# Optimization experiments

Measured on AMD Instinct MI355X. Metric: run time of the kernel, lower is better.

## Reference

```python
import jax, jax.numpy as jnp
import numpy as np

NUM_TASKS = 8
NUM_EXPERTS = 8
TOPK = 2
WEX = 0.01
N_TOKENS = 4194304


def setup_inputs() -> dict:
    key = jax.random.key(0)
    k1, k2 = jax.random.split(key)
    router_logits = jax.random.normal(k1, (N_TOKENS, NUM_EXPERTS), dtype=jnp.float32)
    router_labels = jax.random.randint(k2, (N_TOKENS,), 0, NUM_TASKS, dtype=jnp.int64)
    return {"router_logits": router_logits, "router_labels": router_labels}


def reference(router_logits, router_labels):
    # call_update: detached softmax over experts
    probs = jax.lax.stop_gradient(
        jax.nn.softmax(router_logits.astype(jnp.float32), axis=-1)
    )  # [N, E]
    labels = router_labels.astype(jnp.int32)
    # Torch loop `for task in router_labels` adds segment_sum[task] once per
    # occurrence of task -> EX_task_gate[t] = count[t] * segment_sum[t]
    seg_sum = jax.ops.segment_sum(probs, labels, num_segments=NUM_TASKS)  # [T, E]
    counts = jax.ops.segment_sum(
        jnp.ones((probs.shape[0],), dtype=jnp.float32), labels, num_segments=NUM_TASKS
    )  # [T]
    EX_gate = seg_sum * counts[:, None]  # [T, E]
    # calculate_mutual_information_loss
    tot = EX_gate.sum() / TOPK
    EX_gate = EX_gate / (tot + 0.0001)
    P_TI = EX_gate.sum(axis=1, keepdims=True) + 0.0001  # [T, 1]
    P_EI = EX_gate.sum(axis=0, keepdims=True) + 0.0001  # [1, E]
    expert_loss = -(EX_gate * jnp.log(EX_gate / P_TI / P_EI + 0.0001)).sum()
    return jnp.float32(WEX) * expert_loss
```

## Files before the change

kernel.cpp:

```cpp
#include <hip/hip_runtime.h>
#include <hip/hip_bf16.h>

#define N_TOKENS    4194304
#define NUM_EXPERTS 8
#define NUM_TASKS   8
#define GRID        2048
#define BLOCK       256
#define NTH         (GRID * BLOCK)
#define HSLOTS      (N_TOKENS * 2 / NTH)
#define PF          4

__global__ __launch_bounds__(BLOCK) void mi_reduce_kernel(
    const float* __restrict__ logits,
    const int*   __restrict__ labels,
    float*       __restrict__ partials) {

  float acc[NUM_TASKS][4];
#pragma unroll
  for (int t = 0; t < NUM_TASKS; ++t)
#pragma unroll
    for (int e = 0; e < 4; ++e) acc[t][e] = 0.0f;

  const int u    = blockIdx.x * BLOCK + threadIdx.x;
  const int tok0 = u >> 1;
  const float4* __restrict__ lp = reinterpret_cast<const float4*>(logits);

  float4 va[PF]; int la[PF];
  float4 vb[PF]; int lb[PF];

#define LOADB(ARR, LARR, B)                                                  \
  _Pragma("unroll")                                                          \
  for (int j = 0; j < PF; ++j) {                                             \
    const int k = (B) * PF + j;                                              \
    (ARR)[j]  = lp[(size_t)k * NTH + u];            \
    (LARR)[j] = labels[k * (NTH / 2) + tok0];               \
  }

#define PROC(ARR, LARR)                                                      \
  _Pragma("unroll")                                                          \
  for (int j = 0; j < PF; ++j) {                                             \
    float4 w = (ARR)[j];                                                     \
    float p0 = __expf(w.x);                                                  \
    float p1 = __expf(w.y);                                                  \
    float p2 = __expf(w.z);                                                  \
    float p3 = __expf(w.w);                                                  \
    float s = (p0 + p1) + (p2 + p3);                                         \
    s += __shfl_xor(s, 1, 64);                   \
    float r = __builtin_amdgcn_rcpf(s);                                      \
    p0 *= r; p1 *= r; p2 *= r; p3 *= r;                                      \
    const int lab = (LARR)[j];                                               \
    _Pragma("unroll")                                                        \
    for (int t = 0; t < NUM_TASKS; ++t) {                                    \
      float m = (lab == t) ? 1.0f : 0.0f;                                    \
      acc[t][0] = fmaf(m, p0, acc[t][0]);                                    \
      acc[t][1] = fmaf(m, p1, acc[t][1]);                                    \
      acc[t][2] = fmaf(m, p2, acc[t][2]);                                    \
      acc[t][3] = fmaf(m, p3, acc[t][3]);                                    \
    }                                                                        \
  }

  LOADB(va, la, 0);
  LOADB(vb, lb, 1);
  __builtin_amdgcn_sched_barrier(0);
  PROC(va, la);
  LOADB(va, la, 2);
  __builtin_amdgcn_sched_barrier(0);
  PROC(vb, lb);
  LOADB(vb, lb, 3);
  __builtin_amdgcn_sched_barrier(0);
  PROC(va, la);
  PROC(vb, lb);

#undef LOADB
#undef PROC

#pragma unroll
  for (int t = 0; t < NUM_TASKS; ++t)
#pragma unroll
    for (int e = 0; e < 4; ++e) {
      float x = acc[t][e];
#pragma unroll
      for (int m = 2; m < 64; m <<= 1) x += __shfl_xor(x, m, 64);
      acc[t][e] = x;
    }

  __shared__ float sacc[64];
  if (threadIdx.x < 64) sacc[threadIdx.x] = 0.0f;
  __syncthreads();
  const int lane = threadIdx.x & 63;
  if (lane < 2) {
    const int eoff = lane * 4;
#pragma unroll
    for (int t = 0; t < NUM_TASKS; ++t)
#pragma unroll
      for (int e = 0; e < 4; ++e)
        atomicAdd(&sacc[t * NUM_EXPERTS + eoff + e], acc[t][e]);
  }
  __syncthreads();
  if (threadIdx.x < 64)
    partials[blockIdx.x * 64 + threadIdx.x] = sacc[threadIdx.x];
}

__global__ __launch_bounds__(1024) void mi_finalize_kernel(
    const float* __restrict__ partials,
    float*       __restrict__ out) {
  __shared__ float red[1024];
  const int tid = threadIdx.x;
  const int c   = tid & 63;
  const int rb  = tid >> 6;

  float s = 0.0f;
#pragma unroll 8
  for (int r = rb; r < GRID; r += 16) s += partials[r * 64 + c];
  red[tid] = s;
  __syncthreads();
  if (tid < 512) red[tid] += red[tid + 512];
  __syncthreads();
  if (tid < 256) red[tid] += red[tid + 256];
  __syncthreads();
  if (tid < 128) red[tid] += red[tid + 128];
  __syncthreads();
  if (tid < 64)  red[tid] += red[tid + 64];
  __syncthreads();

  if (tid < 64) {
    float seg = red[tid];

    float cnt = seg;
    cnt += __shfl_xor(cnt, 1, 64);
    cnt += __shfl_xor(cnt, 2, 64);
    cnt += __shfl_xor(cnt, 4, 64);

    float ex = seg * cnt;

    float tot = ex;
#pragma unroll
    for (int m = 1; m < 64; m <<= 1) tot += __shfl_xor(tot, m, 64);
    tot *= 0.5f;
    ex = ex / (tot + 1e-4f);

    float pti = ex;
    pti += __shfl_xor(pti, 1, 64);
    pti += __shfl_xor(pti, 2, 64);
    pti += __shfl_xor(pti, 4, 64);
    pti += 1e-4f;

    float pei = ex;
    pei += __shfl_xor(pei, 8, 64);
    pei += __shfl_xor(pei, 16, 64);
    pei += __shfl_xor(pei, 32, 64);
    pei += 1e-4f;

    float term = -ex * logf(ex / pti / pei + 1e-4f);
#pragma unroll
    for (int m = 1; m < 64; m <<= 1) term += __shfl_xor(term, m, 64);

    if (tid == 0) out[0] = 0.01f * term;
  }
}

extern "C" void kernel_launch(void* const* d_in, const int* in_sizes, int n_in,
                              void* d_out, int out_size, void* d_ws, size_t ws_size,
                              hipStream_t stream) {
  const float* logits = (const float*)d_in[0];
  const int*   labels = (const int*)d_in[1];
  float* out = (float*)d_out;
  float* partials = (float*)d_ws;

  mi_reduce_kernel<<<GRID, BLOCK, 0, stream>>>(logits, labels, partials);
  mi_finalize_kernel<<<1, 1024, 0, stream>>>(partials, out);
}
```

Baseline: 210.5 us.

## Stage logits through LDS with direct global-to-LDS double-buffered tiles

Each block now owns a contiguous chunk of tokens and streams it in 512-token tiles. The tiles are copied straight into a double-buffered shared-memory array with global_load_lds, and the next tile's labels are prefetched while the current tile is processed. This replaces the strided per-thread register prefetch and aims for contiguous per-block streaming and better overlap of loads with compute. In exchange it adds LDS traffic and a __syncthreads per tile. There is also a possible read-after-write hazard: the code relies on the later barrier to cover completion of the asynchronous LDS loads, with no explicit vmcnt wait.

```diff
diff --git a/kernel.cpp b/kernel.cpp
--- a/kernel.cpp
+++ b/kernel.cpp
@@ -1,19 +1,21 @@
 #include <hip/hip_runtime.h>
-#include <hip/hip_bf16.h>
 
 #define N_TOKENS    4194304
 #define NUM_EXPERTS 8
 #define NUM_TASKS   8
 #define GRID        2048
 #define BLOCK       256
-#define NTH         (GRID * BLOCK)
-#define HSLOTS      (N_TOKENS * 2 / NTH)
-#define PF          4
+#define TPB_TOK     (N_TOKENS / GRID)
+#define TILE_TOK    512
+#define NTILES      (TPB_TOK / TILE_TOK)
+#define TILE_FLOATS (TILE_TOK * NUM_EXPERTS)
 
 __global__ __launch_bounds__(BLOCK) void mi_reduce_kernel(
     const float* __restrict__ logits,
     const int*   __restrict__ labels,
     float*       __restrict__ partials) {
+
+  __shared__ float lbuf[2][TILE_FLOATS];
 
   float acc[NUM_TASKS][4];
 #pragma unroll
@@ -21,37 +23,53 @@
 #pragma unroll
     for (int e = 0; e < 4; ++e) acc[t][e] = 0.0f;
 
-  const int u    = blockIdx.x * BLOCK + threadIdx.x;
-  const int tok0 = u >> 1;
-  const float4* __restrict__ lp = reinterpret_cast<const float4*>(logits);
+  const int tid  = threadIdx.x;
+  const int lane = tid & 63;
+  const int wid  = tid >> 6;
+  const int half = tid & 1;
+  const int trow = tid >> 1;
 
-  float4 va[PF]; int la[PF];
-  float4 vb[PF]; int lb[PF];
+  const size_t blkTok = (size_t)blockIdx.x * TPB_TOK;
 
-#define LOADB(ARR, LARR, B)                                                  \
-  _Pragma("unroll")                                                          \
-  for (int j = 0; j < PF; ++j) {                                             \
-    const int k = (B) * PF + j;                                              \
-    (ARR)[j]  = lp[(size_t)k * NTH + u];            \
-    (LARR)[j] = labels[k * (NTH / 2) + tok0];               \
+  int lab[4], labn[4];
+
+#define STAGE(T, b)                                                          \
+  {                                                                          \
+    const float* gbase =                                                     \
+        logits + (blkTok + (size_t)(T) * TILE_TOK) * NUM_EXPERTS;            \
+    _Pragma("unroll")                                                        \
+    for (int c = 0; c < 4; ++c) {                                            \
+      const int off = (wid * 4 + c) * 256;         \
+      const float* g = gbase + off + lane * 4;            \
+      __builtin_amdgcn_global_load_lds(                                      \
+          (const __attribute__((address_space(1))) void*)g,                  \
+          (__attribute__((address_space(3))) void*)&lbuf[b][off],            \
+          16, 0, 0);                                                         \
+    }                                                                        \
   }
 
-#define PROC(ARR, LARR)                                                      \
+#define LOADLAB(T, DST)                                                      \
+  {                                                                          \
+    const int* lb = labels + blkTok + (T) * TILE_TOK;                        \
+    _Pragma("unroll")                                                        \
+    for (int s = 0; s < 4; ++s) (DST)[s] = lb[s * 128 + trow];               \
+  }
+
+#define PROC(b)                                                              \
   _Pragma("unroll")                                                          \
-  for (int j = 0; j < PF; ++j) {                                             \
-    float4 w = (ARR)[j];                                                     \
-    float p0 = __expf(w.x);                                                  \
-    float p1 = __expf(w.y);                                                  \
-    float p2 = __expf(w.z);                                                  \
-    float p3 = __expf(w.w);                                                  \
-    float s = (p0 + p1) + (p2 + p3);                                         \
-    s += __shfl_xor(s, 1, 64);                   \
-    float r = __builtin_amdgcn_rcpf(s);                                      \
+  for (int s = 0; s < 4; ++s) {                                              \
+    float4 w = *reinterpret_cast<const float4*>(                             \
+        &lbuf[b][s * 1024 + trow * 8 + half * 4]);                           \
+    float p0 = __expf(w.x), p1 = __expf(w.y);                                \
+    float p2 = __expf(w.z), p3 = __expf(w.w);                                \
+    float sum = (p0 + p1) + (p2 + p3);                                       \
+    sum += __shfl_xor(sum, 1, 64);                    \
+    float r = __builtin_amdgcn_rcpf(sum);                                    \
     p0 *= r; p1 *= r; p2 *= r; p3 *= r;                                      \
-    const int lab = (LARR)[j];                                               \
+    const int lb_ = lab[s];                                                  \
     _Pragma("unroll")                                                        \
     for (int t = 0; t < NUM_TASKS; ++t) {                                    \
-      float m = (lab == t) ? 1.0f : 0.0f;                                    \
+      float m = (lb_ == t) ? 1.0f : 0.0f;                                    \
       acc[t][0] = fmaf(m, p0, acc[t][0]);                                    \
       acc[t][1] = fmaf(m, p1, acc[t][1]);                                    \
       acc[t][2] = fmaf(m, p2, acc[t][2]);                                    \
@@ -59,19 +77,27 @@
     }                                                                        \
   }
 
-  LOADB(va, la, 0);
-  LOADB(vb, lb, 1);
-  __builtin_amdgcn_sched_barrier(0);
-  PROC(va, la);
-  LOADB(va, la, 2);
-  __builtin_amdgcn_sched_barrier(0);
-  PROC(vb, lb);
-  LOADB(vb, lb, 3);
-  __builtin_amdgcn_sched_barrier(0);
-  PROC(va, la);
-  PROC(vb, lb);
+  STAGE(0, 0);
+  LOADLAB(0, lab);
+  __syncthreads();
 
-#undef LOADB
+  int cur = 0;
+#pragma unroll
+  for (int T = 0; T < NTILES; ++T) {
+    if (T + 1 < NTILES) {
+      STAGE(T + 1, cur ^ 1);
+      LOADLAB(T + 1, labn);
+      __builtin_amdgcn_sched_barrier(0);
+    }
+    PROC(cur);
+    __syncthreads();
+    cur ^= 1;
+#pragma unroll
+    for (int s = 0; s < 4; ++s) lab[s] = labn[s];
+  }
+
+#undef STAGE
+#undef LOADLAB
 #undef PROC
 
 #pragma unroll
@@ -84,10 +110,9 @@
       acc[t][e] = x;
     }
 
-  __shared__ float sacc[64];
-  if (threadIdx.x < 64) sacc[threadIdx.x] = 0.0f;
+  float* sacc = &lbuf[0][0];
+  if (tid < 64) sacc[tid] = 0.0f;
   __syncthreads();
-  const int lane = threadIdx.x & 63;
   if (lane < 2) {
     const int eoff = lane * 4;
 #pragma unroll
@@ -97,8 +122,8 @@
         atomicAdd(&sacc[t * NUM_EXPERTS + eoff + e], acc[t][e]);
   }
   __syncthreads();
-  if (threadIdx.x < 64)
-    partials[blockIdx.x * 64 + threadIdx.x] = sacc[threadIdx.x];
+  if (tid < 64)
+    partials[blockIdx.x * 64 + tid] = sacc[tid];
 }
 
 __global__ __launch_bounds__(1024) void mi_finalize_kernel(
```

New measurement: 212.4 us. Within noise of the previous version (+0.9%).
